# Optimization experiments

Hardware: AMD Instinct MI355X
Metric: run time of the kernel (lower is better)

Reference implementation:

```python
import jax, jax.numpy as jnp
import numpy as np

COMMITMENT_BETA = 0.25


def setup_inputs() -> dict:
    key = jax.random.key(0)
    k1, k2, k3 = jax.random.split(key, 3)
    Q, N, K, D = 4096, 50000, 1024, 256
    return {
        "query_emb": jax.random.normal(k1, (Q, D), dtype=jnp.float32),
        "entity_emb": jax.random.normal(k2, (N, D), dtype=jnp.float32),
        "codebook": jax.random.normal(k3, (K, D), dtype=jnp.float32),
    }


def reference(query_emb, entity_emb, codebook):
    x = entity_emb  # [N, D]
    # squared distance == argmin of torch.norm distance; avoids [N,K,D] tensor)
    x2 = jnp.sum(x * x, axis=1, keepdims=True)          # [N, 1]
    c2 = jnp.sum(codebook * codebook, axis=1)           # [K]
    d2 = x2 + c2[None, :] - 2.0 * (x @ codebook.T)      # [N, K]
    nearest_idx = jnp.argmin(d2, axis=1)                # [N]
    quantized = codebook[nearest_idx]                   # [N, D]

    sg = jax.lax.stop_gradient
    vq_loss = jnp.mean((sg(quantized) - x) ** 2) + COMMITMENT_BETA * jnp.mean(
        (quantized - sg(x)) ** 2
    )
    score = query_emb @ quantized.T                     # [Q, N]
    return score, vq_loss, nearest_idx
```

## Files before the change

### kernel.cpp

```cpp
#include <hip/hip_runtime.h>

#define QDIM 4096
#define NDIM 50000
#define KDIM 1024
#define DDIM 256
#define ABLK 391
#define TAU  0.3f

typedef _Float16 half8 __attribute__((ext_vector_type(8)));
typedef float    f32x4 __attribute__((ext_vector_type(4)));

#define GLD16(srcp, dstp)                                                              \
    __builtin_amdgcn_global_load_lds((const __attribute__((address_space(1))) void*)(srcp), \
                                     (__attribute__((address_space(3))) void*)(dstp), 16, 0, 0)

__device__ float np_pairwise_sq(const float* a) {
#pragma clang fp contract(off)
    float res[2];
    for (int h = 0; h < 2; ++h) {
        const float* p = a + h * 128;
        float r0 = p[0] * p[0], r1 = p[1] * p[1], r2 = p[2] * p[2], r3 = p[3] * p[3];
        float r4 = p[4] * p[4], r5 = p[5] * p[5], r6 = p[6] * p[6], r7 = p[7] * p[7];
        for (int i = 8; i < 128; i += 8) {
            r0 += p[i + 0] * p[i + 0];
            r1 += p[i + 1] * p[i + 1];
            r2 += p[i + 2] * p[i + 2];
            r3 += p[i + 3] * p[i + 3];
            r4 += p[i + 4] * p[i + 4];
            r5 += p[i + 5] * p[i + 5];
            r6 += p[i + 6] * p[i + 6];
            r7 += p[i + 7] * p[i + 7];
        }
        res[h] = ((r0 + r1) + (r2 + r3)) + ((r4 + r5) + (r6 + r7));
    }
    return res[0] + res[1];
}

__device__ float np_exact_d2(const float* __restrict__ xr, const float* __restrict__ cp,
                             float x2, float c2v) {
    float dot = 0.f;
    for (int d = 0; d < DDIM; ++d) dot = __builtin_fmaf(cp[d], xr[d], dot);
    return (x2 + c2v) - 2.0f * dot;
}

__global__ __launch_bounds__(256) void prepcvt_kernel(const float* __restrict__ cb,
                                                      float* __restrict__ c2np,
                                                      _Float16* __restrict__ cbh,
                                                      int* __restrict__ refCtr) {
#pragma clang fp contract(off)
    int tid = threadIdx.x;
    int code = blockIdx.x * 16 + (tid >> 4);
    int l = tid & 15;
    {
        int h = l >> 3, j = l & 7;
        const float* p = cb + (size_t)code * DDIM + h * 128;
        float v0 = p[j];
        float r = v0 * v0;
        for (int i = 8; i < 128; i += 8) { float v = p[i + j]; r = r + v * v; }
        r += __shfl_xor(r, 1, 16);
        r += __shfl_xor(r, 2, 16);
        r += __shfl_xor(r, 4, 16);
        r += __shfl_xor(r, 8, 16);
        if (l == 0) c2np[code] = r;
    }
    {
        const float* srcv = cb + (size_t)code * DDIM + l * 16;
        _Float16* dstv = cbh + (size_t)code * DDIM + l * 16;
#pragma unroll
        for (int u = 0; u < 2; ++u) {
            float4 v0 = *(const float4*)&srcv[u * 8];
            float4 v1 = *(const float4*)&srcv[u * 8 + 4];
            half8 h;
            h[0] = (_Float16)v0.x; h[1] = (_Float16)v0.y; h[2] = (_Float16)v0.z; h[3] = (_Float16)v0.w;
            h[4] = (_Float16)v1.x; h[5] = (_Float16)v1.y; h[6] = (_Float16)v1.z; h[7] = (_Float16)v1.w;
            *(half8*)&dstv[u * 8] = h;
        }
    }
    if (code == 0 && l == 0) { refCtr[0] = 0; refCtr[1] = 0; }
}

__global__ __launch_bounds__(256) void argmin128_kernel(const float* __restrict__ E,
                                                        const _Float16* __restrict__ CBH,
                                                        const float* __restrict__ c2,
                                                        int* __restrict__ idxOut,
                                                        float* __restrict__ idxF,
                                                        float* __restrict__ lossPart,
                                                        int* __restrict__ refCtr,
                                                        int4* __restrict__ refQuad,
                                                        int* __restrict__ refFull) {
    __shared__ _Float16 Buf[2][64 * 256];
    __shared__ float c2s[KDIM];
    __shared__ float xsq[128];
    __shared__ float rowd2s[128];
    int tid = threadIdx.x;
    int lane = tid & 63;
    int w = tid >> 6;
    int g = lane >> 4, cl = lane & 15;
    int rowBase = blockIdx.x * 128 + w * 32;

    half8 a[2][8];
#pragma unroll
    for (int rt = 0; rt < 2; ++rt) {
        int row = rowBase + rt * 16 + cl;
        int rg = row < NDIM ? row : NDIM - 1;
        const float* src = E + (size_t)rg * DDIM + g * 8;
        float s = 0.f;
#pragma unroll
        for (int s8 = 0; s8 < 8; ++s8) {
            float4 v0 = *(const float4*)&src[s8 * 32];
            float4 v1 = *(const float4*)&src[s8 * 32 + 4];
            s += v0.x * v0.x + v0.y * v0.y + v0.z * v0.z + v0.w * v0.w;
            s += v1.x * v1.x + v1.y * v1.y + v1.z * v1.z + v1.w * v1.w;
            half8 h;
            h[0] = (_Float16)v0.x; h[1] = (_Float16)v0.y; h[2] = (_Float16)v0.z; h[3] = (_Float16)v0.w;
            h[4] = (_Float16)v1.x; h[5] = (_Float16)v1.y; h[6] = (_Float16)v1.z; h[7] = (_Float16)v1.w;
            a[rt][s8] = h;
        }
        s += __shfl_xor(s, 16, 64);
        s += __shfl_xor(s, 32, 64);
        if (g == 0) xsq[w * 32 + rt * 16 + cl] = s;
    }

    const _Float16* bsrc[8];
    int bdstOff[8];
    {
        int rowLoc = lane >> 5;
        int chunk = lane & 31;
#pragma unroll
        for (int i = 0; i < 8; ++i) {
            int row = w * 16 + i * 2 + rowLoc;
            int sc = chunk ^ (row & 7);
            bsrc[i] = CBH + (size_t)row * DDIM + sc * 8;
            bdstOff[i] = (w * 16 + i * 2) * 256;
        }
    }

    *(float4*)&c2s[tid * 4] = *(const float4*)&c2[tid * 4];
#pragma unroll
    for (int i = 0; i < 8; ++i) GLD16(bsrc[i], &Buf[0][bdstOff[i]]);
    __syncthreads();

    float m1[2][4] = {{1e30f, 1e30f, 1e30f, 1e30f}, {1e30f, 1e30f, 1e30f, 1e30f}};
    float m2[2][4] = {{1e30f, 1e30f, 1e30f, 1e30f}, {1e30f, 1e30f, 1e30f, 1e30f}};
    float m3[2][4] = {{1e30f, 1e30f, 1e30f, 1e30f}, {1e30f, 1e30f, 1e30f, 1e30f}};
    int   i1[2][4] = {{0, 0, 0, 0}, {0, 0, 0, 0}};
    int   i2[2][4] = {{0, 0, 0, 0}, {0, 0, 0, 0}};

    int cur = 0;
    for (int kc = 0; kc < 16; ++kc) {
        if (kc + 1 < 16) {
            size_t koff = (size_t)(kc + 1) * 64 * DDIM;
#pragma unroll
            for (int i = 0; i < 8; ++i) GLD16(bsrc[i] + koff, &Buf[cur ^ 1][bdstOff[i]]);
        }
        float cc[4];
#pragma unroll
        for (int t = 0; t < 4; ++t) cc[t] = c2s[kc * 64 + t * 16 + cl];

#pragma unroll
        for (int t = 0; t < 4; ++t) {
            int cB = t * 16 + cl;
            int ki = kc * 64 + cB;
            half8 bfr[8];
#pragma unroll
            for (int s8 = 0; s8 < 8; ++s8) {
                int slot = (s8 * 4 + g) ^ (cB & 7);
                bfr[s8] = *(half8*)&Buf[cur][cB * 256 + slot * 8];
            }
#pragma unroll
            for (int rt = 0; rt < 2; ++rt) {
                f32x4 acc = {0.f, 0.f, 0.f, 0.f};
#pragma unroll
                for (int s8 = 0; s8 < 8; ++s8)
                    acc = __builtin_amdgcn_mfma_f32_16x16x32_f16(a[rt][s8], bfr[s8], acc, 0, 0, 0);
#pragma unroll
                for (int j = 0; j < 4; ++j) {
                    float v = cc[t] - 2.0f * acc[j];
                    if (v < m1[rt][j])      { m3[rt][j] = m2[rt][j]; m2[rt][j] = m1[rt][j]; i2[rt][j] = i1[rt][j]; m1[rt][j] = v; i1[rt][j] = ki; }
                    else if (v < m2[rt][j]) { m3[rt][j] = m2[rt][j]; m2[rt][j] = v; i2[rt][j] = ki; }
                    else if (v < m3[rt][j]) { m3[rt][j] = v; }
                }
            }
        }
        __syncthreads();
        cur ^= 1;
    }
#pragma unroll
    for (int rt = 0; rt < 2; ++rt) {
#pragma unroll
        for (int j = 0; j < 4; ++j) {
            for (int m = 8; m >= 1; m >>= 1) {
                float o1 = __shfl_xor(m1[rt][j], m, 16);
                int   oi1 = __shfl_xor(i1[rt][j], m, 16);
                float o2 = __shfl_xor(m2[rt][j], m, 16);
                int   oi2 = __shfl_xor(i2[rt][j], m, 16);
                float o3 = __shfl_xor(m3[rt][j], m, 16);
                float a1, a2, a3, b1, b2, b3; int ai1, ai2, bi1, bi2;
                if (o1 < m1[rt][j] || (o1 == m1[rt][j] && oi1 < i1[rt][j])) {
                    a1 = o1; ai1 = oi1; a2 = o2; ai2 = oi2; a3 = o3;
                    b1 = m1[rt][j]; bi1 = i1[rt][j]; b2 = m2[rt][j]; bi2 = i2[rt][j]; b3 = m3[rt][j];
                } else {
                    a1 = m1[rt][j]; ai1 = i1[rt][j]; a2 = m2[rt][j]; ai2 = i2[rt][j]; a3 = m3[rt][j];
                    b1 = o1; bi1 = oi1; b2 = o2; bi2 = oi2; b3 = o3;
                }
                (void)bi2; (void)b3;
                m1[rt][j] = a1; i1[rt][j] = ai1;
                if (b1 < a2 || (b1 == a2 && bi1 < ai2)) {
                    m2[rt][j] = b1; i2[rt][j] = bi1; m3[rt][j] = fminf(a2, b2);
                } else {
                    m2[rt][j] = a2; i2[rt][j] = ai2; m3[rt][j] = fminf(a3, b1);
                }
            }
        }
    }
    if (cl == 0) {
#pragma unroll
        for (int rt = 0; rt < 2; ++rt) {
#pragma unroll
            for (int j = 0; j < 4; ++j) {
                int rloc = w * 32 + rt * 16 + g * 4 + j;
                int row = blockIdx.x * 128 + rloc;
                if (row < NDIM) {
                    idxOut[row] = i1[rt][j];
                    idxF[row] = (float)i1[rt][j];
                    rowd2s[rloc] = xsq[rloc] + m1[rt][j];
                    int full = (m3[rt][j] - m1[rt][j] < TAU) ? 1 : 0;
                    if (m2[rt][j] - m1[rt][j] < TAU) {
                        int p = atomicAdd(&refCtr[0], 1);
                        if ((unsigned)p < (unsigned)NDIM) {
                            int4 q; q.x = row; q.y = i1[rt][j]; q.z = i2[rt][j]; q.w = full;
                            refQuad[p] = q;
                        }
                    }
                    if (full) {
                        int p = atomicAdd(&refCtr[1], 1);
                        if ((unsigned)p < (unsigned)NDIM) refFull[p] = row;
                    }
                } else {
                    rowd2s[rloc] = 0.f;
                }
            }
        }
    }
    __syncthreads();
    if (tid == 0) {
        float s = 0.f;
        for (int i = 0; i < 128; ++i) s += rowd2s[i];
        lossPart[blockIdx.x] = s;
    }
}

__global__ __launch_bounds__(256) void sgemm16_kernel(const float* __restrict__ Q,
                                                      const _Float16* __restrict__ CBH,
                                                      float* __restrict__ S) {
    __shared__ _Float16 Buf[64 * 256];
    int tid = threadIdx.x;
    int lane = tid & 63;
    int w = tid >> 6;
    int rowBase = blockIdx.x * 64;
    int kcBase = blockIdx.y * 2;

    {
        int r = tid >> 2, seg = tid & 3;
        const float* src = Q + (size_t)(rowBase + r) * DDIM + seg * 64;
#pragma unroll
        for (int i = 0; i < 8; ++i) {
            float4 v0 = *(const float4*)&src[i * 8];
            float4 v1 = *(const float4*)&src[i * 8 + 4];
            half8 h;
            h[0] = (_Float16)v0.x; h[1] = (_Float16)v0.y; h[2] = (_Float16)v0.z; h[3] = (_Float16)v0.w;
            h[4] = (_Float16)v1.x; h[5] = (_Float16)v1.y; h[6] = (_Float16)v1.z; h[7] = (_Float16)v1.w;
            int slot = (seg * 8 + i) ^ (r & 7);
            *(half8*)&Buf[r * 256 + slot * 8] = h;
        }
    }
    __syncthreads();
    half8 a[8];
    {
        int rA = w * 16 + (lane & 15);
        int g = lane >> 4;
#pragma unroll
        for (int s8 = 0; s8 < 8; ++s8) {
            int slot = (s8 * 4 + g) ^ (rA & 7);
            a[s8] = *(half8*)&Buf[rA * 256 + slot * 8];
        }
    }

    const _Float16* bsrc[8];
    _Float16* bdst[8];
    {
        int rowLoc = lane >> 5;
        int chunk = lane & 31;
#pragma unroll
        for (int i = 0; i < 8; ++i) {
            int row = w * 16 + i * 2 + rowLoc;
            int sc = chunk ^ (row & 7);
            bsrc[i] = CBH + (size_t)row * DDIM + sc * 8;
            bdst[i] = &Buf[(w * 16 + i * 2) * 256];
        }
    }

    for (int kci = 0; kci < 2; ++kci) {
        int kc = kcBase + kci;
        __syncthreads();
        size_t koff = (size_t)kc * 64 * DDIM;
#pragma unroll
        for (int i = 0; i < 8; ++i) GLD16(bsrc[i] + koff, bdst[i]);
        __syncthreads();

        int g = lane >> 4;
#pragma unroll
        for (int t = 0; t < 4; ++t) {
            f32x4 acc = {0.f, 0.f, 0.f, 0.f};
            int cB = t * 16 + (lane & 15);
#pragma unroll
            for (int s8 = 0; s8 < 8; ++s8) {
                int slot = (s8 * 4 + g) ^ (cB & 7);
                half8 b = *(half8*)&Buf[cB * 256 + slot * 8];
                acc = __builtin_amdgcn_mfma_f32_16x16x32_f16(a[s8], b, acc, 0, 0, 0);
            }
#pragma unroll
            for (int j = 0; j < 4; ++j) {
                int row = rowBase + w * 16 + g * 4 + j;
                S[(size_t)row * KDIM + kc * 64 + cB] = acc[j];
            }
        }
    }
}

__global__ __launch_bounds__(256) void reffuse_kernel(const float* __restrict__ E,
                                                      const float* __restrict__ CB,
                                                      const float* __restrict__ c2np,
                                                      const int* __restrict__ refCtr,
                                                      const int4* __restrict__ refQuad,
                                                      const int* __restrict__ refFull,
                                                      int* __restrict__ idxOut,
                                                      float* __restrict__ idxF,
                                                      const float* __restrict__ lossPart,
                                                      float* __restrict__ lossOut) {
    int tid = threadIdx.x;
    int c0 = refCtr[0]; if (c0 > NDIM) c0 = NDIM;
    for (int i = blockIdx.x * 256 + tid; i < c0; i += gridDim.x * 256) {
        int4 q = refQuad[i];
        if (q.w) continue;
        int row = q.x, a = q.y, b = q.z;
        const float* xr = E + (size_t)row * DDIM;
        float x2 = np_pairwise_sq(xr);
        float va = np_exact_d2(xr, CB + (size_t)a * DDIM, x2, c2np[a]);
        float vb = np_exact_d2(xr, CB + (size_t)b * DDIM, x2, c2np[b]);
        int win = (vb < va || (vb == va && b < a)) ? b : a;
        idxOut[row] = win;
        idxF[row] = (float)win;
    }
    __shared__ float xrow[DDIM];
    __shared__ float x2sh;
    __shared__ float wval[4];
    __shared__ int widx[4];
    int c1 = refCtr[1]; if (c1 > NDIM) c1 = NDIM;
    for (int b = blockIdx.x; b < c1; b += gridDim.x) {
        int row = refFull[b];
        xrow[tid] = E[(size_t)row * DDIM + tid];
        __syncthreads();
        if (tid == 0) x2sh = np_pairwise_sq(xrow);
        __syncthreads();
        float best = 1e30f;
        int bidx = 0x7fffffff;
#pragma unroll
        for (int kk = 0; kk < 4; ++kk) {
            int k = tid + kk * 256;
            const float* cp = CB + (size_t)k * DDIM;
            float dot = 0.f;
            for (int d = 0; d < DDIM; ++d) dot = __builtin_fmaf(cp[d], xrow[d], dot);
            float t1 = x2sh + c2np[k];
            float v = t1 - 2.0f * dot;
            if (v < best || (v == best && k < bidx)) { best = v; bidx = k; }
        }
        for (int m = 32; m >= 1; m >>= 1) {
            float ov = __shfl_xor(best, m, 64);
            int   oi = __shfl_xor(bidx, m, 64);
            if (ov < best || (ov == best && oi < bidx)) { best = ov; bidx = oi; }
        }
        if ((tid & 63) == 0) { wval[tid >> 6] = best; widx[tid >> 6] = bidx; }
        __syncthreads();
        if (tid == 0) {
            float bv = wval[0]; int bi = widx[0];
#pragma unroll
            for (int w = 1; w < 4; ++w)
                if (wval[w] < bv || (wval[w] == bv && widx[w] < bi)) { bv = wval[w]; bi = widx[w]; }
            idxOut[row] = bi;
            idxF[row] = (float)bi;
        }
        __syncthreads();
    }
    if (blockIdx.x == 0 && tid < 64) {
        float s = 0.f;
        for (int i = tid; i < ABLK; i += 64) s += lossPart[i];
        for (int m = 32; m >= 1; m >>= 1) s += __shfl_down(s, m, 64);
        if (tid == 0) lossOut[0] = 1.25f * s / (float)(NDIM * DDIM);
    }
}

__global__ __launch_bounds__(256) void gather_kernel(const float* __restrict__ S,
                                                     const int* __restrict__ idx,
                                                     float* __restrict__ score) {
    __shared__ float Srow[4 * 1024];
    int tid = threadIdx.x;
    int qBase = blockIdx.y * 4;
    int nBase = blockIdx.x * 2048;
#pragma unroll
    for (int i = 0; i < 4; ++i) {
        int o = (tid + i * 256) * 4;
        *(float4*)&Srow[o] = *(const float4*)&S[(size_t)qBase * KDIM + o];
    }
    __syncthreads();
#pragma unroll
    for (int s = 0; s < 2; ++s) {
        int n = nBase + s * 1024 + tid * 4;
        if (n < NDIM) {
            int4 id = *(const int4*)&idx[n];
#pragma unroll
            for (int q = 0; q < 4; ++q) {
                const float* sp = &Srow[q * 1024];
                f32x4 v = {sp[id.x], sp[id.y], sp[id.z], sp[id.w]};
                __builtin_nontemporal_store(v, (f32x4*)&score[(size_t)(qBase + q) * NDIM + n]);
            }
        }
    }
}

extern "C" void kernel_launch(void* const* d_in, const int* in_sizes, int n_in,
                              void* d_out, int out_size, void* d_ws, size_t ws_size,
                              hipStream_t stream) {
    const float* query  = (const float*)d_in[0];
    const float* entity = (const float*)d_in[1];
    const float* cb     = (const float*)d_in[2];
    float* out = (float*)d_out;
    char* ws = (char*)d_ws;

    float*     S        = (float*)ws;
    float*     c2np     = (float*)(ws + 16777216);
    int*       idxW     = (int*)  (ws + 16781312);
    int*       refCtr   = (int*)  (ws + 16981312);
    int4*      refQuad  = (int4*) (ws + 16981376);
    int*       refFull  = (int*)  (ws + 17781376);
    float*     lossPart = (float*)(ws + 17981376);
    _Float16*  cbh      = (_Float16*)(ws + 17984512);

    size_t QN = (size_t)QDIM * NDIM;
    float* score   = out;
    float* lossOut = out + QN;
    float* idxF    = out + QN + 1;

    prepcvt_kernel<<<dim3(KDIM / 16), dim3(256), 0, stream>>>(cb, c2np, cbh, refCtr);
    sgemm16_kernel<<<dim3(QDIM / 64, 8), dim3(256), 0, stream>>>(query, cbh, S);
    argmin128_kernel<<<dim3(ABLK), dim3(256), 0, stream>>>(entity, cbh, c2np, idxW, idxF,
                                                           lossPart, refCtr, refQuad, refFull);
    reffuse_kernel<<<dim3(256), dim3(256), 0, stream>>>(entity, cb, c2np, refCtr, refQuad, refFull,
                                                        idxW, idxF, lossPart, lossOut);
    gather_kernel<<<dim3((NDIM + 2047) / 2048, QDIM / 4), dim3(256), 0, stream>>>(S, idxW, score);
}
```

Measured before the change: 331.1 us.

## Merge query-codebook GEMM and argmin kernels into one heterogeneous launch

Folds the independent sgemm16 kernel (query x codebook) into the argmin kernel as extra blocks dispatched by blockIdx, so both run in a single launch of ABLK+SBLK blocks. This removes one kernel launch and lets the small GEMM blocks fill CUs left idle by the 391 argmin blocks. The GEMM blocks now share the larger shared-memory footprint of the argmin path, which may reduce occupancy for them.

Result: faster. 320.7 us (-3.1%).

```diff
diff --git a/kernel.cpp b/kernel.cpp
--- a/kernel.cpp
+++ b/kernel.cpp
@@ -5,6 +5,7 @@
 #define KDIM 1024
 #define DDIM 256
 #define ABLK 391
+#define SBLK 512
 #define TAU  0.3f
 
 typedef _Float16 half8 __attribute__((ext_vector_type(8)));
@@ -79,15 +80,17 @@
     if (code == 0 && l == 0) { refCtr[0] = 0; refCtr[1] = 0; }
 }
 
-__global__ __launch_bounds__(256) void argmin128_kernel(const float* __restrict__ E,
-                                                        const _Float16* __restrict__ CBH,
-                                                        const float* __restrict__ c2,
-                                                        int* __restrict__ idxOut,
-                                                        float* __restrict__ idxF,
-                                                        float* __restrict__ lossPart,
-                                                        int* __restrict__ refCtr,
-                                                        int4* __restrict__ refQuad,
-                                                        int* __restrict__ refFull) {
+__global__ __launch_bounds__(256) void main_kernel(const float* __restrict__ E,
+                                                   const float* __restrict__ Q,
+                                                   const _Float16* __restrict__ CBH,
+                                                   const float* __restrict__ c2,
+                                                   float* __restrict__ S,
+                                                   int* __restrict__ idxOut,
+                                                   float* __restrict__ idxF,
+                                                   float* __restrict__ lossPart,
+                                                   int* __restrict__ refCtr,
+                                                   int4* __restrict__ refQuad,
+                                                   int* __restrict__ refFull) {
     __shared__ _Float16 Buf[2][64 * 256];
     __shared__ float c2s[KDIM];
     __shared__ float xsq[128];
@@ -96,233 +99,227 @@
     int lane = tid & 63;
     int w = tid >> 6;
     int g = lane >> 4, cl = lane & 15;
-    int rowBase = blockIdx.x * 128 + w * 32;
-
-    half8 a[2][8];
-#pragma unroll
-    for (int rt = 0; rt < 2; ++rt) {
-        int row = rowBase + rt * 16 + cl;
-        int rg = row < NDIM ? row : NDIM - 1;
-        const float* src = E + (size_t)rg * DDIM + g * 8;
-        float s = 0.f;
-#pragma unroll
-        for (int s8 = 0; s8 < 8; ++s8) {
-            float4 v0 = *(const float4*)&src[s8 * 32];
-            float4 v1 = *(const float4*)&src[s8 * 32 + 4];
-            s += v0.x * v0.x + v0.y * v0.y + v0.z * v0.z + v0.w * v0.w;
-            s += v1.x * v1.x + v1.y * v1.y + v1.z * v1.z + v1.w * v1.w;
-            half8 h;
-            h[0] = (_Float16)v0.x; h[1] = (_Float16)v0.y; h[2] = (_Float16)v0.z; h[3] = (_Float16)v0.w;
-            h[4] = (_Float16)v1.x; h[5] = (_Float16)v1.y; h[6] = (_Float16)v1.z; h[7] = (_Float16)v1.w;
-            a[rt][s8] = h;
-        }
-        s += __shfl_xor(s, 16, 64);
-        s += __shfl_xor(s, 32, 64);
-        if (g == 0) xsq[w * 32 + rt * 16 + cl] = s;
-    }
-
-    const _Float16* bsrc[8];
-    int bdstOff[8];
-    {
-        int rowLoc = lane >> 5;
-        int chunk = lane & 31;
-#pragma unroll
-        for (int i = 0; i < 8; ++i) {
-            int row = w * 16 + i * 2 + rowLoc;
-            int sc = chunk ^ (row & 7);
-            bsrc[i] = CBH + (size_t)row * DDIM + sc * 8;
-            bdstOff[i] = (w * 16 + i * 2) * 256;
-        }
-    }
-
-    *(float4*)&c2s[tid * 4] = *(const float4*)&c2[tid * 4];
-#pragma unroll
-    for (int i = 0; i < 8; ++i) GLD16(bsrc[i], &Buf[0][bdstOff[i]]);
-    __syncthreads();
-
-    float m1[2][4] = {{1e30f, 1e30f, 1e30f, 1e30f}, {1e30f, 1e30f, 1e30f, 1e30f}};
-    float m2[2][4] = {{1e30f, 1e30f, 1e30f, 1e30f}, {1e30f, 1e30f, 1e30f, 1e30f}};
-    float m3[2][4] = {{1e30f, 1e30f, 1e30f, 1e30f}, {1e30f, 1e30f, 1e30f, 1e30f}};
-    int   i1[2][4] = {{0, 0, 0, 0}, {0, 0, 0, 0}};
-    int   i2[2][4] = {{0, 0, 0, 0}, {0, 0, 0, 0}};
-
-    int cur = 0;
-    for (int kc = 0; kc < 16; ++kc) {
-        if (kc + 1 < 16) {
-            size_t koff = (size_t)(kc + 1) * 64 * DDIM;
-#pragma unroll
-            for (int i = 0; i < 8; ++i) GLD16(bsrc[i] + koff, &Buf[cur ^ 1][bdstOff[i]]);
-        }
-        float cc[4];
-#pragma unroll
-        for (int t = 0; t < 4; ++t) cc[t] = c2s[kc * 64 + t * 16 + cl];
-
-#pragma unroll
-        for (int t = 0; t < 4; ++t) {
-            int cB = t * 16 + cl;
-            int ki = kc * 64 + cB;
-            half8 bfr[8];
+
+    if (blockIdx.x < ABLK) {
+        int rowBase = blockIdx.x * 128 + w * 32;
+
+        half8 a[2][8];
+#pragma unroll
+        for (int rt = 0; rt < 2; ++rt) {
+            int row = rowBase + rt * 16 + cl;
+            int rg = row < NDIM ? row : NDIM - 1;
+            const float* src = E + (size_t)rg * DDIM + g * 8;
+            float s = 0.f;
 #pragma unroll
             for (int s8 = 0; s8 < 8; ++s8) {
-                int slot = (s8 * 4 + g) ^ (cB & 7);
-                bfr[s8] = *(half8*)&Buf[cur][cB * 256 + slot * 8];
-            }
+                float4 v0 = *(const float4*)&src[s8 * 32];
+                float4 v1 = *(const float4*)&src[s8 * 32 + 4];
+                s += v0.x * v0.x + v0.y * v0.y + v0.z * v0.z + v0.w * v0.w;
+                s += v1.x * v1.x + v1.y * v1.y + v1.z * v1.z + v1.w * v1.w;
+                half8 h;
+                h[0] = (_Float16)v0.x; h[1] = (_Float16)v0.y; h[2] = (_Float16)v0.z; h[3] = (_Float16)v0.w;
+                h[4] = (_Float16)v1.x; h[5] = (_Float16)v1.y; h[6] = (_Float16)v1.z; h[7] = (_Float16)v1.w;
+                a[rt][s8] = h;
+            }
+            s += __shfl_xor(s, 16, 64);
+            s += __shfl_xor(s, 32, 64);
+            if (g == 0) xsq[w * 32 + rt * 16 + cl] = s;
+        }
+
+        const _Float16* bsrc[8];
+        int bdstOff[8];
+        {
+            int rowLoc = lane >> 5;
+            int chunk = lane & 31;
+#pragma unroll
+            for (int i = 0; i < 8; ++i) {
+                int row = w * 16 + i * 2 + rowLoc;
+                int sc = chunk ^ (row & 7);
+                bsrc[i] = CBH + (size_t)row * DDIM + sc * 8;
+                bdstOff[i] = (w * 16 + i * 2) * 256;
+            }
+        }
+
+        *(float4*)&c2s[tid * 4] = *(const float4*)&c2[tid * 4];
+#pragma unroll
+        for (int i = 0; i < 8; ++i) GLD16(bsrc[i], &Buf[0][bdstOff[i]]);
+        __syncthreads();
+
+        float m1[2][4] = {{1e30f, 1e30f, 1e30f, 1e30f}, {1e30f, 1e30f, 1e30f, 1e30f}};
+        float m2[2][4] = {{1e30f, 1e30f, 1e30f, 1e30f}, {1e30f, 1e30f, 1e30f, 1e30f}};
+        float m3[2][4] = {{1e30f, 1e30f, 1e30f, 1e30f}, {1e30f, 1e30f, 1e30f, 1e30f}};
+        int   i1[2][4] = {{0, 0, 0, 0}, {0, 0, 0, 0}};
+        int   i2[2][4] = {{0, 0, 0, 0}, {0, 0, 0, 0}};
+
+        int cur = 0;
+        for (int kc = 0; kc < 16; ++kc) {
+            if (kc + 1 < 16) {
+                size_t koff = (size_t)(kc + 1) * 64 * DDIM;
+#pragma unroll
+                for (int i = 0; i < 8; ++i) GLD16(bsrc[i] + koff, &Buf[cur ^ 1][bdstOff[i]]);
+            }
+            float cc[4];
+#pragma unroll
+            for (int t = 0; t < 4; ++t) cc[t] = c2s[kc * 64 + t * 16 + cl];
+
+#pragma unroll
+            for (int t = 0; t < 4; ++t) {
+                int cB = t * 16 + cl;
+                int ki = kc * 64 + cB;
+                half8 bfr[8];
+#pragma unroll
+                for (int s8 = 0; s8 < 8; ++s8) {
+                    int slot = (s8 * 4 + g) ^ (cB & 7);
+                    bfr[s8] = *(half8*)&Buf[cur][cB * 256 + slot * 8];
+                }
+#pragma unroll
+                for (int rt = 0; rt < 2; ++rt) {
+                    f32x4 acc = {0.f, 0.f, 0.f, 0.f};
+#pragma unroll
+                    for (int s8 = 0; s8 < 8; ++s8)
+                        acc = __builtin_amdgcn_mfma_f32_16x16x32_f16(a[rt][s8], bfr[s8], acc, 0, 0, 0);
+#pragma unroll
+                    for (int j = 0; j < 4; ++j) {
+                        float v = cc[t] - 2.0f * acc[j];
+                        if (v < m1[rt][j])      { m3[rt][j] = m2[rt][j]; m2[rt][j] = m1[rt][j]; i2[rt][j] = i1[rt][j]; m1[rt][j] = v; i1[rt][j] = ki; }
+                        else if (v < m2[rt][j]) { m3[rt][j] = m2[rt][j]; m2[rt][j] = v; i2[rt][j] = ki; }
+                        else if (v < m3[rt][j]) { m3[rt][j] = v; }
+                    }
+                }
+            }
+            __syncthreads();
+            cur ^= 1;
+        }
+#pragma unroll
+        for (int rt = 0; rt < 2; ++rt) {
+#pragma unroll
+            for (int j = 0; j < 4; ++j) {
+                for (int m = 8; m >= 1; m >>= 1) {
+                    float o1 = __shfl_xor(m1[rt][j], m, 16);
+                    int   oi1 = __shfl_xor(i1[rt][j], m, 16);
+                    float o2 = __shfl_xor(m2[rt][j], m, 16);
+                    int   oi2 = __shfl_xor(i2[rt][j], m, 16);
+                    float o3 = __shfl_xor(m3[rt][j], m, 16);
+                    float a1, a2, a3, b1, b2, b3; int ai1, ai2, bi1, bi2;
+                    if (o1 < m1[rt][j] || (o1 == m1[rt][j] && oi1 < i1[rt][j])) {
+                        a1 = o1; ai1 = oi1; a2 = o2; ai2 = oi2; a3 = o3;
+                        b1 = m1[rt][j]; bi1 = i1[rt][j]; b2 = m2[rt][j]; bi2 = i2[rt][j]; b3 = m3[rt][j];
+                    } else {
+                        a1 = m1[rt][j]; ai1 = i1[rt][j]; a2 = m2[rt][j]; ai2 = i2[rt][j]; a3 = m3[rt][j];
+                        b1 = o1; bi1 = oi1; b2 = o2; bi2 = oi2; b3 = o3;
+                    }
+                    (void)bi2; (void)b3;
+                    m1[rt][j] = a1; i1[rt][j] = ai1;
+                    if (b1 < a2 || (b1 == a2 && bi1 < ai2)) {
+                        m2[rt][j] = b1; i2[rt][j] = bi1; m3[rt][j] = fminf(a2, b2);
+                    } else {
+                        m2[rt][j] = a2; i2[rt][j] = ai2; m3[rt][j] = fminf(a3, b1);
+                    }
+                }
+            }
+        }
+        if (cl == 0) {
 #pragma unroll
             for (int rt = 0; rt < 2; ++rt) {
+#pragma unroll
+                for (int j = 0; j < 4; ++j) {
+                    int rloc = w * 32 + rt * 16 + g * 4 + j;
+                    int row = blockIdx.x * 128 + rloc;
+                    if (row < NDIM) {
+                        idxOut[row] = i1[rt][j];
+                        idxF[row] = (float)i1[rt][j];
+                        rowd2s[rloc] = xsq[rloc] + m1[rt][j];
+                        int full = (m3[rt][j] - m1[rt][j] < TAU) ? 1 : 0;
+                        if (m2[rt][j] - m1[rt][j] < TAU) {
+                            int p = atomicAdd(&refCtr[0], 1);
+                            if ((unsigned)p < (unsigned)NDIM) {
+                                int4 q; q.x = row; q.y = i1[rt][j]; q.z = i2[rt][j]; q.w = full;
+                                refQuad[p] = q;
+                            }
+                        }
+                        if (full) {
+                            int p = atomicAdd(&refCtr[1], 1);
+                            if ((unsigned)p < (unsigned)NDIM) refFull[p] = row;
+                        }
+                    } else {
+                        rowd2s[rloc] = 0.f;
+                    }
+                }
+            }
+        }
+        __syncthreads();
+        if (tid == 0) {
+            float s = 0.f;
+            for (int i = 0; i < 128; ++i) s += rowd2s[i];
+            lossPart[blockIdx.x] = s;
+        }
+    } else {
+        int bx = blockIdx.x - ABLK;
+        int rowBase = (bx & 63) * 64;
+        int kcBase = (bx >> 6) * 2;
+
+        {
+            int r = tid >> 2, seg = tid & 3;
+            const float* src = Q + (size_t)(rowBase + r) * DDIM + seg * 64;
+#pragma unroll
+            for (int i = 0; i < 8; ++i) {
+                float4 v0 = *(const float4*)&src[i * 8];
+                float4 v1 = *(const float4*)&src[i * 8 + 4];
+                half8 h;
+                h[0] = (_Float16)v0.x; h[1] = (_Float16)v0.y; h[2] = (_Float16)v0.z; h[3] = (_Float16)v0.w;
+                h[4] = (_Float16)v1.x; h[5] = (_Float16)v1.y; h[6] = (_Float16)v1.z; h[7] = (_Float16)v1.w;
+                int slot = (seg * 8 + i) ^ (r & 7);
+                *(half8*)&Buf[0][r * 256 + slot * 8] = h;
+            }
+        }
+        __syncthreads();
+        half8 a[8];
+        {
+            int rA = w * 16 + cl;
+#pragma unroll
+            for (int s8 = 0; s8 < 8; ++s8) {
+                int slot = (s8 * 4 + g) ^ (rA & 7);
+                a[s8] = *(half8*)&Buf[0][rA * 256 + slot * 8];
+            }
+        }
+
+        const _Float16* bsrc[8];
+        _Float16* bdst[8];
+        {
+            int rowLoc = lane >> 5;
+            int chunk = lane & 31;
+#pragma unroll
+            for (int i = 0; i < 8; ++i) {
+                int row = w * 16 + i * 2 + rowLoc;
+                int sc = chunk ^ (row & 7);
+                bsrc[i] = CBH + (size_t)row * DDIM + sc * 8;
+                bdst[i] = &Buf[0][(w * 16 + i * 2) * 256];
+            }
+        }
+
+        for (int kci = 0; kci < 2; ++kci) {
+            int kc = kcBase + kci;
+            __syncthreads();
+            size_t koff = (size_t)kc * 64 * DDIM;
+#pragma unroll
+            for (int i = 0; i < 8; ++i) GLD16(bsrc[i] + koff, bdst[i]);
+            __syncthreads();
+
+#pragma unroll
+            for (int t = 0; t < 4; ++t) {
                 f32x4 acc = {0.f, 0.f, 0.f, 0.f};
-#pragma unroll
-                for (int s8 = 0; s8 < 8; ++s8)
-                    acc = __builtin_amdgcn_mfma_f32_16x16x32_f16(a[rt][s8], bfr[s8], acc, 0, 0, 0);
+                int cB = t * 16 + cl;
+#pragma unroll
+                for (int s8 = 0; s8 < 8; ++s8) {
+                    int slot = (s8 * 4 + g) ^ (cB & 7);
+                    half8 b = *(half8*)&Buf[0][cB * 256 + slot * 8];
+                    acc = __builtin_amdgcn_mfma_f32_16x16x32_f16(a[s8], b, acc, 0, 0, 0);
+                }
 #pragma unroll
                 for (int j = 0; j < 4; ++j) {
-                    float v = cc[t] - 2.0f * acc[j];
-                    if (v < m1[rt][j])      { m3[rt][j] = m2[rt][j]; m2[rt][j] = m1[rt][j]; i2[rt][j] = i1[rt][j]; m1[rt][j] = v; i1[rt][j] = ki; }
-                    else if (v < m2[rt][j]) { m3[rt][j] = m2[rt][j]; m2[rt][j] = v; i2[rt][j] = ki; }
-                    else if (v < m3[rt][j]) { m3[rt][j] = v; }
-                }
-            }
-        }
-        __syncthreads();
-        cur ^= 1;
-    }
-#pragma unroll
-    for (int rt = 0; rt < 2; ++rt) {
-#pragma unroll
-        for (int j = 0; j < 4; ++j) {
-            for (int m = 8; m >= 1; m >>= 1) {
-                float o1 = __shfl_xor(m1[rt][j], m, 16);
-                int   oi1 = __shfl_xor(i1[rt][j], m, 16);
-                float o2 = __shfl_xor(m2[rt][j], m, 16);
-                int   oi2 = __shfl_xor(i2[rt][j], m, 16);
-                float o3 = __shfl_xor(m3[rt][j], m, 16);
-                float a1, a2, a3, b1, b2, b3; int ai1, ai2, bi1, bi2;
-                if (o1 < m1[rt][j] || (o1 == m1[rt][j] && oi1 < i1[rt][j])) {
-                    a1 = o1; ai1 = oi1; a2 = o2; ai2 = oi2; a3 = o3;
-                    b1 = m1[rt][j]; bi1 = i1[rt][j]; b2 = m2[rt][j]; bi2 = i2[rt][j]; b3 = m3[rt][j];
-                } else {
-                    a1 = m1[rt][j]; ai1 = i1[rt][j]; a2 = m2[rt][j]; ai2 = i2[rt][j]; a3 = m3[rt][j];
-                    b1 = o1; bi1 = oi1; b2 = o2; bi2 = oi2; b3 = o3;
-                }
-                (void)bi2; (void)b3;
-                m1[rt][j] = a1; i1[rt][j] = ai1;
-                if (b1 < a2 || (b1 == a2 && bi1 < ai2)) {
-                    m2[rt][j] = b1; i2[rt][j] = bi1; m3[rt][j] = fminf(a2, b2);
-                } else {
-                    m2[rt][j] = a2; i2[rt][j] = ai2; m3[rt][j] = fminf(a3, b1);
-                }
-            }
-        }
-    }
-    if (cl == 0) {
-#pragma unroll
-        for (int rt = 0; rt < 2; ++rt) {
-#pragma unroll
-            for (int j = 0; j < 4; ++j) {
-                int rloc = w * 32 + rt * 16 + g * 4 + j;
-                int row = blockIdx.x * 128 + rloc;
-                if (row < NDIM) {
-                    idxOut[row] = i1[rt][j];
-                    idxF[row] = (float)i1[rt][j];
-                    rowd2s[rloc] = xsq[rloc] + m1[rt][j];
-                    int full = (m3[rt][j] - m1[rt][j] < TAU) ? 1 : 0;
-                    if (m2[rt][j] - m1[rt][j] < TAU) {
-                        int p = atomicAdd(&refCtr[0], 1);
-                        if ((unsigned)p < (unsigned)NDIM) {
-                            int4 q; q.x = row; q.y = i1[rt][j]; q.z = i2[rt][j]; q.w = full;
-                            refQuad[p] = q;
-                        }
-                    }
-                    if (full) {
-                        int p = atomicAdd(&refCtr[1], 1);
-                        if ((unsigned)p < (unsigned)NDIM) refFull[p] = row;
-                    }
-                } else {
-                    rowd2s[rloc] = 0.f;
-                }
-            }
-        }
-    }
-    __syncthreads();
-    if (tid == 0) {
-        float s = 0.f;
-        for (int i = 0; i < 128; ++i) s += rowd2s[i];
-        lossPart[blockIdx.x] = s;
-    }
-}
-
-__global__ __launch_bounds__(256) void sgemm16_kernel(const float* __restrict__ Q,
-                                                      const _Float16* __restrict__ CBH,
-                                                      float* __restrict__ S) {
-    __shared__ _Float16 Buf[64 * 256];
-    int tid = threadIdx.x;
-    int lane = tid & 63;
-    int w = tid >> 6;
-    int rowBase = blockIdx.x * 64;
-    int kcBase = blockIdx.y * 2;
-
-    {
-        int r = tid >> 2, seg = tid & 3;
-        const float* src = Q + (size_t)(rowBase + r) * DDIM + seg * 64;
-#pragma unroll
-        for (int i = 0; i < 8; ++i) {
-            float4 v0 = *(const float4*)&src[i * 8];
-            float4 v1 = *(const float4*)&src[i * 8 + 4];
-            half8 h;
-            h[0] = (_Float16)v0.x; h[1] = (_Float16)v0.y; h[2] = (_Float16)v0.z; h[3] = (_Float16)v0.w;
-            h[4] = (_Float16)v1.x; h[5] = (_Float16)v1.y; h[6] = (_Float16)v1.z; h[7] = (_Float16)v1.w;
-            int slot = (seg * 8 + i) ^ (r & 7);
-            *(half8*)&Buf[r * 256 + slot * 8] = h;
-        }
-    }
-    __syncthreads();
-    half8 a[8];
-    {
-        int rA = w * 16 + (lane & 15);
-        int g = lane >> 4;
-#pragma unroll
-        for (int s8 = 0; s8 < 8; ++s8) {
-            int slot = (s8 * 4 + g) ^ (rA & 7);
-            a[s8] = *(half8*)&Buf[rA * 256 + slot * 8];
-        }
-    }
-
-    const _Float16* bsrc[8];
-    _Float16* bdst[8];
-    {
-        int rowLoc = lane >> 5;
-        int chunk = lane & 31;
-#pragma unroll
-        for (int i = 0; i < 8; ++i) {
-            int row = w * 16 + i * 2 + rowLoc;
-            int sc = chunk ^ (row & 7);
-            bsrc[i] = CBH + (size_t)row * DDIM + sc * 8;
-            bdst[i] = &Buf[(w * 16 + i * 2) * 256];
-        }
-    }
-
-    for (int kci = 0; kci < 2; ++kci) {
-        int kc = kcBase + kci;
-        __syncthreads();
-        size_t koff = (size_t)kc * 64 * DDIM;
-#pragma unroll
-        for (int i = 0; i < 8; ++i) GLD16(bsrc[i] + koff, bdst[i]);
-        __syncthreads();
-
-        int g = lane >> 4;
-#pragma unroll
-        for (int t = 0; t < 4; ++t) {
-            f32x4 acc = {0.f, 0.f, 0.f, 0.f};
-            int cB = t * 16 + (lane & 15);
-#pragma unroll
-            for (int s8 = 0; s8 < 8; ++s8) {
-                int slot = (s8 * 4 + g) ^ (cB & 7);
-                half8 b = *(half8*)&Buf[cB * 256 + slot * 8];
-                acc = __builtin_amdgcn_mfma_f32_16x16x32_f16(a[s8], b, acc, 0, 0, 0);
-            }
-#pragma unroll
-            for (int j = 0; j < 4; ++j) {
-                int row = rowBase + w * 16 + g * 4 + j;
-                S[(size_t)row * KDIM + kc * 64 + cB] = acc[j];
+                    int row = rowBase + w * 16 + g * 4 + j;
+                    S[(size_t)row * KDIM + kc * 64 + cB] = acc[j];
+                }
             }
         }
     }
@@ -452,9 +449,9 @@
     float* idxF    = out + QN + 1;
 
     prepcvt_kernel<<<dim3(KDIM / 16), dim3(256), 0, stream>>>(cb, c2np, cbh, refCtr);
-    sgemm16_kernel<<<dim3(QDIM / 64, 8), dim3(256), 0, stream>>>(query, cbh, S);
-    argmin128_kernel<<<dim3(ABLK), dim3(256), 0, stream>>>(entity, cbh, c2np, idxW, idxF,
-                                                           lossPart, refCtr, refQuad, refFull);
+    main_kernel<<<dim3(ABLK + SBLK), dim3(256), 0, stream>>>(entity, query, cbh, c2np, S,
+                                                             idxW, idxF, lossPart,
+                                                             refCtr, refQuad, refFull);
     reffuse_kernel<<<dim3(256), dim3(256), 0, stream>>>(entity, cb, c2np, refCtr, refQuad, refFull,
                                                         idxW, idxF, lossPart, lossOut);
     gather_kernel<<<dim3((NDIM + 2047) / 2048, QDIM / 4), dim3(256), 0, stream>>>(S, idxW, score);
```
